# Optimization experiments

Measured on AMD Instinct MI355X. Metric: run time of the kernel, lower is better.

Reference implementation:

```python
import jax, jax.numpy as jnp
import numpy as np

N, F, K, O = 8192, 512, 2, 64
FMIN = jnp.finfo(jnp.float32).min


def setup_inputs() -> dict:
    key = jax.random.key(0)
    k1, k2, k3, k4, k5 = jax.random.split(key, 5)
    H = jax.random.normal(k1, (N, F), dtype=jnp.float32)
    # sparse-ish binary adjacency with self-loops (float mask, as in TF code)
    A = (jax.random.uniform(k2, (N, N)) < 0.0125).astype(jnp.float32)
    A = jnp.maximum(A, jnp.eye(N, dtype=jnp.float32))
    idx = jnp.arange(N, dtype=jnp.int32)
    W = jax.random.normal(k3, (K, F, O), dtype=jnp.float32) * 0.1
    b = jnp.zeros((K, O), dtype=jnp.float32)
    a1 = jax.random.normal(k4, (K, O), dtype=jnp.float32) * 0.1
    a2 = jax.random.normal(k5, (K, O), dtype=jnp.float32) * 0.1
    return {"H": H, "A": A, "idx": idx, "W": W, "b": b, "a1": a1, "a2": a2}


def reference(H, A, idx, W, b, a1, a2):
    # batch_A = tf.gather(A, idx, axis=1)
    batch_A = A[:, idx]                                  # [N, N]
    HW = jnp.einsum('nf,kfo->kno', H, W)                 # [K, N, O]
    attn1 = jnp.einsum('kno,ko->kn', HW, a1)             # [K, N]
    attn2 = jnp.einsum('kno,ko->kn', HW, a2)             # [K, N]
    # transpose(meshgrid sum): scores[k, i, j] = attn1[k, i] + attn2[k, j]
    scores = attn1[:, :, None] + attn2[:, None, :]       # [K, N, N]
    scores = scores + FMIN * (1.0 - batch_A)[None]
    scores = jnp.where(scores >= 0, scores, 0.2 * scores)  # LeakyReLU(0.2)
    attn = jax.nn.softmax(scores, axis=-1)               # [K, N, N]
    # res = transpose(HW^T @ attn) => res[k, i] = sum_j attn[k, j, i] * HW[k, j]
    res = jnp.einsum('kji,kjo->kio', attn, HW)           # [K, N, O]
    out = jax.nn.relu(res + b[:, None, :])               # [K, N, O]
    # concat heads along feature axis
    return jnp.transpose(out, (1, 0, 2)).reshape(N, K * O)
```

## Files before the change

### kernel.cpp

```cpp
#include <hip/hip_runtime.h>

#define NN 8192
#define FD 512
typedef unsigned long long u64;

__device__ __forceinline__ unsigned f2bf(float x) {
  unsigned u = __float_as_uint(x);
  u += 0x7FFFu + ((u >> 16) & 1u);
  return u >> 16;
}

__device__ __forceinline__ int flt2key(float f) {
  int i = __float_as_int(f);
  return i >= 0 ? i : (i ^ 0x7FFFFFFF);
}
__device__ __forceinline__ float key2flt(int k) {
  return __int_as_float(k >= 0 ? k : (k ^ 0x7FFFFFFF));
}

__device__ __forceinline__ int col0_of_word(int w) {
  return ((w >> 5) << 11) + (((w >> 2) & 7) << 8) + (w & 3);
}

__global__ __launch_bounds__(256) void k1_hw(
    const float* __restrict__ H, const float* __restrict__ W,
    const float* __restrict__ a1, const float* __restrict__ a2,
    const int* __restrict__ idx, int* __restrict__ flag,
    unsigned short* __restrict__ hw2, float* __restrict__ c1, float* __restrict__ c2p,
    int* __restrict__ gkey) {
  if (blockIdx.x >= 512) {
    const int t = (blockIdx.x - 512) * 256 + threadIdx.x;
    int4 v = ((const int4*)idx)[t];
    const int base = t * 4;
    bool bad = (v.x != base) | (v.y != base + 1) | (v.z != base + 2) | (v.w != base + 3);
    const bool any = (__ballot(bad) != 0ULL);
    if ((threadIdx.x & 63) == 0) atomicMax(flag, any ? 1 : 0);
    return;
  }
  const int k    = blockIdx.x & 1;
  const int wv   = threadIdx.x >> 6;
  const int lane = threadIdx.x & 63;
  const int nbase = __builtin_amdgcn_readfirstlane((blockIdx.x >> 1) * 32 + wv * 8);
  const float* __restrict__ Wk = W + k * (FD * 64);
  float acc[8] = {0.f,0.f,0.f,0.f,0.f,0.f,0.f,0.f};
  for (int f = 0; f < FD; f += 4) {
    float w0 = Wk[(f+0)*64 + lane];
    float w1 = Wk[(f+1)*64 + lane];
    float w2 = Wk[(f+2)*64 + lane];
    float w3 = Wk[(f+3)*64 + lane];
#pragma unroll
    for (int r = 0; r < 8; ++r) {
      float4 h = *(const float4*)(H + (size_t)(nbase + r) * FD + f);
      acc[r] = fmaf(h.x, w0, acc[r]);
      acc[r] = fmaf(h.y, w1, acc[r]);
      acc[r] = fmaf(h.z, w2, acc[r]);
      acc[r] = fmaf(h.w, w3, acc[r]);
    }
  }
  const float a1v = a1[k*64 + lane];
  const float a2v = a2[k*64 + lane];
  float wmax = -3.4e38f;
#pragma unroll
  for (int r = 0; r < 8; ++r) {
    const int n = nbase + r;
    hw2[((size_t)n * 64 + lane) * 2 + k] = (unsigned short)f2bf(acc[r]);
    float t1 = acc[r] * a1v;
    float t2 = acc[r] * a2v;
#pragma unroll
    for (int off = 32; off; off >>= 1) {
      t1 += __shfl_down(t1, off);
      t2 += __shfl_down(t2, off);
    }
    if (lane == 0) {
      c1[k*NN + n] = t1;
      c2p[n*2 + k] = t2;
      wmax = fmaxf(wmax, t2);
    }
  }
  if (lane == 0) atomicMax(&gkey[k], flt2key(wmax));
}

__global__ __launch_bounds__(256) void k2_scan(
    const float* __restrict__ A, const int* __restrict__ idx, const int* __restrict__ flag,
    const int* __restrict__ gkey,
    const float* __restrict__ c1, const float* __restrict__ c2p,
    u64* __restrict__ mask, float4* __restrict__ param2) {
  __shared__ u64 sm[128];
  __shared__ float redl[2][4];
  const int tid = threadIdx.x;
  const int wv = tid >> 6, lane = tid & 63;
  const int j = (NN - 1) - blockIdx.x;
  const bool fast = (flag[0] == 0);
  const float* __restrict__ Arow = A + (size_t)j * NN;

  float4 a[8];
  if (fast) {
#pragma unroll
    for (int p = 0; p < 8; ++p)
      a[p] = *(const float4*)(Arow + wv * 2048 + p * 256 + lane * 4);
  } else {
#pragma unroll
    for (int p = 0; p < 8; ++p) {
      const int c0 = wv * 2048 + p * 256 + lane * 4;
      a[p].x = Arow[idx[c0+0]]; a[p].y = Arow[idx[c0+1]];
      a[p].z = Arow[idx[c0+2]]; a[p].w = Arow[idx[c0+3]];
    }
  }
#pragma unroll
  for (int p = 0; p < 8; ++p) {
    const float av[4] = {a[p].x, a[p].y, a[p].z, a[p].w};
#pragma unroll
    for (int c = 0; c < 4; ++c) {
      const u64 bal = __ballot(av[c] != 0.f);
      if (lane == 0) sm[wv * 32 + p * 4 + c] = bal;
    }
  }
  __syncthreads();
  if (tid < 64) {
    ulonglong2 v;
    v.x = sm[tid * 2];
    v.y = sm[tid * 2 + 1];
    *(ulonglong2*)(mask + (size_t)j * 128 + tid * 2) = v;
  }
  const float c10 = c1[j];
  const float c11 = c1[NN + j];
  float M0 = c10 + key2flt(gkey[0]); M0 = (M0 >= 0.f) ? M0 : 0.2f * M0;
  float M1 = c11 + key2flt(gkey[1]); M1 = (M1 >= 0.f) ? M1 : 0.2f * M1;
  float s0 = 0.f, s1 = 0.f;
  if (tid < 128) {
    u64 m = sm[tid];
    const int cb = col0_of_word(tid);
    while (m) {
      int b[4] = {0, 0, 0, 0};
      int n = 1;
      b[0] = __builtin_ctzll(m); m &= m - 1;
      if (m) { b[1] = __builtin_ctzll(m); m &= m - 1; n = 2;
        if (m) { b[2] = __builtin_ctzll(m); m &= m - 1; n = 3;
          if (m) { b[3] = __builtin_ctzll(m); m &= m - 1; n = 4; } } }
      float2 cv[4];
#pragma unroll
      for (int q = 0; q < 4; ++q)
        cv[q] = *(const float2*)(c2p + (cb + 4 * b[q]) * 2);
#pragma unroll
      for (int q = 0; q < 4; ++q) {
        if (q < n) {
          float v0 = c10 + cv[q].x; v0 = (v0 >= 0.f) ? v0 : 0.2f * v0;
          s0 += __expf(v0 - M0);
          float v1 = c11 + cv[q].y; v1 = (v1 >= 0.f) ? v1 : 0.2f * v1;
          s1 += __expf(v1 - M1);
        }
      }
    }
  }
#pragma unroll
  for (int off = 32; off; off >>= 1) {
    s0 += __shfl_down(s0, off);
    s1 += __shfl_down(s1, off);
  }
  if (lane == 0) { redl[0][wv] = s0; redl[1][wv] = s1; }
  __syncthreads();
  if (tid == 0) {
    float S0 = redl[0][0] + redl[0][1] + redl[0][2] + redl[0][3];
    float S1 = redl[1][0] + redl[1][1] + redl[1][2] + redl[1][3];
    const float I0 = (S0 > 0.f) ? 1.f / S0 : 0.f;
    const float I1 = (S1 > 0.f) ? 1.f / S1 : 0.f;
    param2[j*2 + 0] = make_float4(c10, (S0 > 0.f) ? M0 : 0.f, I0, 0.f);
    param2[j*2 + 1] = make_float4(c11, (S1 > 0.f) ? M1 : 0.f, I1, 0.f);
  }
}

__device__ __forceinline__ u64 xpose64(u64 x, int lane) {
  const u64 M[6] = {0x00000000FFFFFFFFULL, 0x0000FFFF0000FFFFULL,
                    0x00FF00FF00FF00FFULL, 0x0F0F0F0F0F0F0F0FULL,
                    0x3333333333333333ULL, 0x5555555555555555ULL};
  int d = 32;
#pragma unroll
  for (int s = 0; s < 6; ++s, d >>= 1) {
    u64 y = __shfl_xor(x, d);
    const u64 ML = M[s], MH = ~ML;
    if ((lane & d) == 0) x = (x & ML) | ((y & ML) << d);
    else                 x = (x & MH) | ((y & MH) >> d);
  }
  return x;
}

__global__ __launch_bounds__(256) void kT(
    const u64* __restrict__ mask, unsigned short* __restrict__ edges16,
    int* __restrict__ ecnt4) {
  __shared__ unsigned short seg[4][32][66];
  __shared__ int scnt[4][64];
  const int wv = threadIdx.x >> 6, lane = threadIdx.x & 63;
  const int w  = blockIdx.x;
  const int qq = blockIdx.y;
  const int jst = qq * 2048 + wv * 512;
  int cnt = 0;
#pragma unroll 1
  for (int jt = 0; jt < 8; jt += 4) {
    u64 x[4];
#pragma unroll
    for (int t = 0; t < 4; ++t)
      x[t] = mask[(size_t)(jst + (jt + t) * 64 + lane) * 128 + w];
#pragma unroll
    for (int t = 0; t < 4; ++t) x[t] = xpose64(x[t], lane);
#pragma unroll
    for (int t = 0; t < 4; ++t) {
      u64 m = x[t];
      const int jb = jst + (jt + t) * 64;
      while (m) {
        const int r = __builtin_ctzll(m);
        m &= m - 1;
        if (cnt < 32) seg[wv][cnt][lane] = (unsigned short)(jb + r);
        ++cnt;
      }
    }
  }
  scnt[wv][lane] = min(cnt, 32);
  __syncthreads();
  for (int rr = 0; rr < 16; ++rr) {
    const int r = wv * 16 + rr;
    const int i = col0_of_word(w) + 4 * r;
    const int c0 = scnt[0][r], c1 = scnt[1][r], c2 = scnt[2][r], c3 = scnt[3][r];
    const int o1 = c0, o2 = o1 + c1, o3 = o2 + c2;
    const int tot = min(o3 + c3, 64);
    const int pos = lane;
    if (pos < tot) {
      int s, off;
      if (pos < o1)      { s = 0; off = pos; }
      else if (pos < o2) { s = 1; off = pos - o1; }
      else if (pos < o3) { s = 2; off = pos - o2; }
      else               { s = 3; off = pos - o3; }
      edges16[(size_t)i * 256 + qq * 64 + pos] = seg[s][off][r];
    }
    if (lane == 0) ecnt4[i * 4 + qq] = tot;
  }
}

__global__ __launch_bounds__(256) void k3_aggregate(
    const int* __restrict__ ecnt4, const unsigned short* __restrict__ edges16,
    const float4* __restrict__ param2, const float* __restrict__ c2p,
    const unsigned* __restrict__ hw2, const float* __restrict__ b,
    float* __restrict__ out) {
  __shared__ unsigned short ebuf[4][256];
  const int wv = threadIdx.x >> 6, lane = threadIdx.x & 63;
  const int i = __builtin_amdgcn_readfirstlane(blockIdx.x * 4 + wv);
  const float c20 = c2p[i*2];
  const float c21 = c2p[i*2 + 1];
  const int4 ec = *(const int4*)(ecnt4 + i * 4);
  const unsigned short* __restrict__ e16 = edges16 + (size_t)i * 256;
  int off = 0;
  {
    if (lane < ec.x) ebuf[wv][off + lane] = e16[lane];            off += ec.x;
    if (lane < ec.y) ebuf[wv][off + lane] = e16[64 + lane];       off += ec.y;
    if (lane < ec.z) ebuf[wv][off + lane] = e16[128 + lane];      off += ec.z;
    if (lane < ec.w) ebuf[wv][off + lane] = e16[192 + lane];      off += ec.w;
  }
  __syncthreads();
  const int cnt = off;
  float acc0 = 0.f, acc1 = 0.f;
  int t = 0;
  for (; t + 8 <= cnt; t += 8) {
    const ushort4 j1 = *(const ushort4*)(&ebuf[wv][t]);
    const ushort4 j2 = *(const ushort4*)(&ebuf[wv][t + 4]);
    const int jj[8] = {j1.x, j1.y, j1.z, j1.w, j2.x, j2.y, j2.z, j2.w};
    float4 p0[8], p1[8];
    unsigned uu[8];
#pragma unroll
    for (int s = 0; s < 8; ++s) {
      p0[s] = param2[jj[s]*2];
      p1[s] = param2[jj[s]*2 + 1];
      uu[s] = hw2[(size_t)jj[s] * 64 + lane];
    }
#pragma unroll
    for (int s = 0; s < 8; ++s) {
      float v, w;
      v = p0[s].x + c20; v = (v >= 0.f) ? v : 0.2f*v; w = __expf(v - p0[s].y) * p0[s].z;
      acc0 = fmaf(w, __uint_as_float(uu[s] << 16), acc0);
      v = p1[s].x + c21; v = (v >= 0.f) ? v : 0.2f*v; w = __expf(v - p1[s].y) * p1[s].z;
      acc1 = fmaf(w, __uint_as_float(uu[s] & 0xFFFF0000u), acc1);
    }
  }
  for (; t < cnt; ++t) {
    const int j = ebuf[wv][t];
    const float4 p0 = param2[j*2], p1 = param2[j*2+1];
    const unsigned u = hw2[(size_t)j * 64 + lane];
    float v0 = p0.x + c20; v0 = (v0 >= 0.f) ? v0 : 0.2f*v0;
    float w0 = __expf(v0 - p0.y) * p0.z;
    float v1 = p1.x + c21; v1 = (v1 >= 0.f) ? v1 : 0.2f*v1;
    float w1 = __expf(v1 - p1.y) * p1.z;
    acc0 = fmaf(w0, __uint_as_float(u << 16), acc0);
    acc1 = fmaf(w1, __uint_as_float(u & 0xFFFF0000u), acc1);
  }
  out[(size_t)i * 128 + lane]      = fmaxf(acc0 + b[lane], 0.f);
  out[(size_t)i * 128 + 64 + lane] = fmaxf(acc1 + b[64 + lane], 0.f);
}

extern "C" void kernel_launch(void* const* d_in, const int* in_sizes, int n_in,
                              void* d_out, int out_size, void* d_ws, size_t ws_size,
                              hipStream_t stream) {
  const float* H   = (const float*)d_in[0];
  const float* A   = (const float*)d_in[1];
  const int*   idx = (const int*)d_in[2];
  const float* W   = (const float*)d_in[3];
  const float* b   = (const float*)d_in[4];
  const float* a1  = (const float*)d_in[5];
  const float* a2  = (const float*)d_in[6];
  float* out = (float*)d_out;

  char* ws = (char*)d_ws;
  unsigned short* hw2     = (unsigned short*)(ws + 0);
  float*          c1      = (float*)(ws + 2097152);
  float*          c2p     = (float*)(ws + 2162688);
  float4*         param2  = (float4*)(ws + 2228224);
  int*            flag    = (int*)(ws + 2490368);
  int*            gkey    = (int*)(ws + 2490372);
  u64*            mask    = (u64*)(ws + 2490624);
  unsigned short* edges16 = (unsigned short*)(ws + 10879232);
  int*            ecnt4   = (int*)(ws + 15073536);

  k1_hw<<<520, 256, 0, stream>>>(H, W, a1, a2, idx, flag, hw2, c1, c2p, gkey);
  k2_scan<<<NN, 256, 0, stream>>>(A, idx, flag, gkey, c1, c2p, mask, param2);
  kT<<<dim3(128, 4), 256, 0, stream>>>(mask, edges16, ecnt4);
  k3_aggregate<<<NN / 4, 256, 0, stream>>>(ecnt4, edges16, param2, c2p, (const unsigned*)hw2, b, out);
}
```

Baseline: 534.2 us.

## Process four adjacency rows per block with register prefetch of the next row

The scan kernel now launches a quarter as many blocks, and each block loops over four rows of A spaced 2048 apart. While it builds the ballot mask for the current row, it loads the next row into a second register buffer, so global-memory latency overlaps with the mask build and the softmax-denominator work. Each block also reads the global max keys once instead of once per row. The costs are extra registers per thread and fewer resident blocks, which could reduce the latency hiding the hardware scheduler already provided.

```diff
diff --git a/kernel.cpp b/kernel.cpp
--- a/kernel.cpp
+++ b/kernel.cpp
@@ -89,83 +89,108 @@
   __shared__ float redl[2][4];
   const int tid = threadIdx.x;
   const int wv = tid >> 6, lane = tid & 63;
-  const int j = (NN - 1) - blockIdx.x;
   const bool fast = (flag[0] == 0);
-  const float* __restrict__ Arow = A + (size_t)j * NN;
-
-  float4 a[8];
-  if (fast) {
-#pragma unroll
-    for (int p = 0; p < 8; ++p)
-      a[p] = *(const float4*)(Arow + wv * 2048 + p * 256 + lane * 4);
-  } else {
+  const float G0 = key2flt(gkey[0]);
+  const float G1 = key2flt(gkey[1]);
+
+  float4 cur[8], nxt[8];
+  int j = blockIdx.x;
+  {
+    const float* __restrict__ Arow = A + (size_t)j * NN;
+    if (fast) {
+#pragma unroll
+      for (int p = 0; p < 8; ++p)
+        cur[p] = *(const float4*)(Arow + wv * 2048 + p * 256 + lane * 4);
+    } else {
+#pragma unroll
+      for (int p = 0; p < 8; ++p) {
+        const int c0 = wv * 2048 + p * 256 + lane * 4;
+        cur[p].x = Arow[idx[c0+0]]; cur[p].y = Arow[idx[c0+1]];
+        cur[p].z = Arow[idx[c0+2]]; cur[p].w = Arow[idx[c0+3]];
+      }
+    }
+  }
+#pragma unroll 1
+  for (int r = 0; r < 4; ++r) {
 #pragma unroll
     for (int p = 0; p < 8; ++p) {
-      const int c0 = wv * 2048 + p * 256 + lane * 4;
-      a[p].x = Arow[idx[c0+0]]; a[p].y = Arow[idx[c0+1]];
-      a[p].z = Arow[idx[c0+2]]; a[p].w = Arow[idx[c0+3]];
-    }
-  }
-#pragma unroll
-  for (int p = 0; p < 8; ++p) {
-    const float av[4] = {a[p].x, a[p].y, a[p].z, a[p].w};
-#pragma unroll
-    for (int c = 0; c < 4; ++c) {
-      const u64 bal = __ballot(av[c] != 0.f);
-      if (lane == 0) sm[wv * 32 + p * 4 + c] = bal;
-    }
-  }
-  __syncthreads();
-  if (tid < 64) {
-    ulonglong2 v;
-    v.x = sm[tid * 2];
-    v.y = sm[tid * 2 + 1];
-    *(ulonglong2*)(mask + (size_t)j * 128 + tid * 2) = v;
-  }
-  const float c10 = c1[j];
-  const float c11 = c1[NN + j];
-  float M0 = c10 + key2flt(gkey[0]); M0 = (M0 >= 0.f) ? M0 : 0.2f * M0;
-  float M1 = c11 + key2flt(gkey[1]); M1 = (M1 >= 0.f) ? M1 : 0.2f * M1;
-  float s0 = 0.f, s1 = 0.f;
-  if (tid < 128) {
-    u64 m = sm[tid];
-    const int cb = col0_of_word(tid);
-    while (m) {
-      int b[4] = {0, 0, 0, 0};
-      int n = 1;
-      b[0] = __builtin_ctzll(m); m &= m - 1;
-      if (m) { b[1] = __builtin_ctzll(m); m &= m - 1; n = 2;
-        if (m) { b[2] = __builtin_ctzll(m); m &= m - 1; n = 3;
-          if (m) { b[3] = __builtin_ctzll(m); m &= m - 1; n = 4; } } }
-      float2 cv[4];
-#pragma unroll
-      for (int q = 0; q < 4; ++q)
-        cv[q] = *(const float2*)(c2p + (cb + 4 * b[q]) * 2);
-#pragma unroll
-      for (int q = 0; q < 4; ++q) {
-        if (q < n) {
-          float v0 = c10 + cv[q].x; v0 = (v0 >= 0.f) ? v0 : 0.2f * v0;
-          s0 += __expf(v0 - M0);
-          float v1 = c11 + cv[q].y; v1 = (v1 >= 0.f) ? v1 : 0.2f * v1;
-          s1 += __expf(v1 - M1);
+      const float av[4] = {cur[p].x, cur[p].y, cur[p].z, cur[p].w};
+#pragma unroll
+      for (int c = 0; c < 4; ++c) {
+        const u64 bal = __ballot(av[c] != 0.f);
+        if (lane == 0) sm[wv * 32 + p * 4 + c] = bal;
+      }
+    }
+    if (r < 3) {
+      const float* __restrict__ Arn = A + (size_t)(j + 2048) * NN;
+      if (fast) {
+#pragma unroll
+        for (int p = 0; p < 8; ++p)
+          nxt[p] = *(const float4*)(Arn + wv * 2048 + p * 256 + lane * 4);
+      } else {
+#pragma unroll
+        for (int p = 0; p < 8; ++p) {
+          const int c0 = wv * 2048 + p * 256 + lane * 4;
+          nxt[p].x = Arn[idx[c0+0]]; nxt[p].y = Arn[idx[c0+1]];
+          nxt[p].z = Arn[idx[c0+2]]; nxt[p].w = Arn[idx[c0+3]];
         }
       }
     }
-  }
-#pragma unroll
-  for (int off = 32; off; off >>= 1) {
-    s0 += __shfl_down(s0, off);
-    s1 += __shfl_down(s1, off);
-  }
-  if (lane == 0) { redl[0][wv] = s0; redl[1][wv] = s1; }
-  __syncthreads();
-  if (tid == 0) {
-    float S0 = redl[0][0] + redl[0][1] + redl[0][2] + redl[0][3];
-    float S1 = redl[1][0] + redl[1][1] + redl[1][2] + redl[1][3];
-    const float I0 = (S0 > 0.f) ? 1.f / S0 : 0.f;
-    const float I1 = (S1 > 0.f) ? 1.f / S1 : 0.f;
-    param2[j*2 + 0] = make_float4(c10, (S0 > 0.f) ? M0 : 0.f, I0, 0.f);
-    param2[j*2 + 1] = make_float4(c11, (S1 > 0.f) ? M1 : 0.f, I1, 0.f);
+    __syncthreads();
+    if (tid < 64) {
+      ulonglong2 v;
+      v.x = sm[tid * 2];
+      v.y = sm[tid * 2 + 1];
+      *(ulonglong2*)(mask + (size_t)j * 128 + tid * 2) = v;
+    }
+    const float c10 = c1[j];
+    const float c11 = c1[NN + j];
+    float M0 = c10 + G0; M0 = (M0 >= 0.f) ? M0 : 0.2f * M0;
+    float M1 = c11 + G1; M1 = (M1 >= 0.f) ? M1 : 0.2f * M1;
+    float s0 = 0.f, s1 = 0.f;
+    if (tid < 128) {
+      u64 m = sm[tid];
+      const int cb = col0_of_word(tid);
+      while (m) {
+        int b[4] = {0, 0, 0, 0};
+        int n = 1;
+        b[0] = __builtin_ctzll(m); m &= m - 1;
+        if (m) { b[1] = __builtin_ctzll(m); m &= m - 1; n = 2;
+          if (m) { b[2] = __builtin_ctzll(m); m &= m - 1; n = 3;
+            if (m) { b[3] = __builtin_ctzll(m); m &= m - 1; n = 4; } } }
+        float2 cv[4];
+#pragma unroll
+        for (int q = 0; q < 4; ++q)
+          cv[q] = *(const float2*)(c2p + (cb + 4 * b[q]) * 2);
+#pragma unroll
+        for (int q = 0; q < 4; ++q) {
+          if (q < n) {
+            float v0 = c10 + cv[q].x; v0 = (v0 >= 0.f) ? v0 : 0.2f * v0;
+            s0 += __expf(v0 - M0);
+            float v1 = c11 + cv[q].y; v1 = (v1 >= 0.f) ? v1 : 0.2f * v1;
+            s1 += __expf(v1 - M1);
+          }
+        }
+      }
+    }
+#pragma unroll
+    for (int off = 32; off; off >>= 1) {
+      s0 += __shfl_down(s0, off);
+      s1 += __shfl_down(s1, off);
+    }
+    if (lane == 0) { redl[0][wv] = s0; redl[1][wv] = s1; }
+    __syncthreads();
+    if (tid == 0) {
+      float S0 = redl[0][0] + redl[0][1] + redl[0][2] + redl[0][3];
+      float S1 = redl[1][0] + redl[1][1] + redl[1][2] + redl[1][3];
+      const float I0 = (S0 > 0.f) ? 1.f / S0 : 0.f;
+      const float I1 = (S1 > 0.f) ? 1.f / S1 : 0.f;
+      param2[j*2 + 0] = make_float4(c10, (S0 > 0.f) ? M0 : 0.f, I0, 0.f);
+      param2[j*2 + 1] = make_float4(c11, (S1 > 0.f) ? M1 : 0.f, I1, 0.f);
+    }
+    j += 2048;
+#pragma unroll
+    for (int p = 0; p < 8; ++p) cur[p] = nxt[p];
   }
 }
 
@@ -318,7 +343,7 @@
   int*            ecnt4   = (int*)(ws + 15073536);
 
   k1_hw<<<520, 256, 0, stream>>>(H, W, a1, a2, idx, flag, hw2, c1, c2p, gkey);
-  k2_scan<<<NN, 256, 0, stream>>>(A, idx, flag, gkey, c1, c2p, mask, param2);
+  k2_scan<<<NN / 4, 256, 0, stream>>>(A, idx, flag, gkey, c1, c2p, mask, param2);
   kT<<<dim3(128, 4), 256, 0, stream>>>(mask, edges16, ecnt4);
   k3_aggregate<<<NN / 4, 256, 0, stream>>>(ecnt4, edges16, param2, c2p, (const unsigned*)hw2, b, out);
 }
```

Result: no change. 537.8 us (+0.7%).
